# Performance work log

Measured on AMD Instinct MI355X. Metric: run time of the kernel, lower is better.

The kernel has to match this reference:

```python
import jax, jax.numpy as jnp
import numpy as np

DIM = 768
HEADS = 12
HEAD_DIM = DIM // HEADS
HIDDEN = 4 * DIM
LS_INIT = 1e-5
EPS = 1e-5


def layernorm(x, g, b):
    mu = jnp.mean(x, axis=-1, keepdims=True)
    var = jnp.mean(jnp.square(x - mu), axis=-1, keepdims=True)
    return (x - mu) * jax.lax.rsqrt(var + EPS) * g + b


def setup_inputs() -> dict:
    key = jax.random.key(0)
    ks = jax.random.split(key, 8)
    s = lambda fan_in: 1.0 / np.sqrt(fan_in)
    return {
        "x": jax.random.normal(ks[0], (8, 1024, DIM), dtype=jnp.float32),
        "ln1_g": jnp.ones((DIM,), jnp.float32),
        "ln1_b": jnp.zeros((DIM,), jnp.float32),
        "w_qkv": jax.random.uniform(ks[1], (3 * DIM, DIM), jnp.float32, -s(DIM), s(DIM)),
        "w_proj": jax.random.uniform(ks[2], (DIM, DIM), jnp.float32, -s(DIM), s(DIM)),
        "b_proj": jnp.zeros((DIM,), jnp.float32),
        "ls1_g": jnp.full((DIM,), LS_INIT, jnp.float32),
        "ln2_g": jnp.ones((DIM,), jnp.float32),
        "ln2_b": jnp.zeros((DIM,), jnp.float32),
        "w_fc1": jax.random.uniform(ks[3], (HIDDEN, DIM), jnp.float32, -s(DIM), s(DIM)),
        "b_fc1": jnp.zeros((HIDDEN,), jnp.float32),
        "w_fc2": jax.random.uniform(ks[4], (DIM, HIDDEN), jnp.float32, -s(HIDDEN), s(HIDDEN)),
        "b_fc2": jnp.zeros((DIM,), jnp.float32),
        "ls2_g": jnp.full((DIM,), LS_INIT, jnp.float32),
    }


def reference(x, ln1_g, ln1_b, w_qkv, w_proj, b_proj, ls1_g,
              ln2_g, ln2_b, w_fc1, b_fc1, w_fc2, b_fc2, ls2_g):
    B, N, C = x.shape
    # --- attention branch ---
    h = layernorm(x, ln1_g, ln1_b)
    qkv = h @ w_qkv.T  # [B,N,3C]
    qkv = qkv.reshape(B, N, 3, HEADS, HEAD_DIM)
    q, k, v = qkv[:, :, 0], qkv[:, :, 1], qkv[:, :, 2]  # [B,N,H,D]
    scale = 1.0 / np.sqrt(HEAD_DIM)
    attn = jnp.einsum("bqhd,bkhd->bhqk", q, k) * scale
    attn = jax.nn.softmax(attn, axis=-1)
    o = jnp.einsum("bhqk,bkhd->bqhd", attn, v).reshape(B, N, C)
    o = o @ w_proj.T + b_proj
    x = x + ls1_g * o
    # --- MLP branch ---
    h = layernorm(x, ln2_g, ln2_b)
    h = jax.nn.gelu(h @ w_fc1.T + b_fc1, approximate=False)
    h = h @ w_fc2.T + b_fc2
    x = x + ls2_g * h
    return x
```

## Files before the change

### kernel.cpp

```cpp
#include <hip/hip_runtime.h>
#include <cstdint>
#include <cstddef>

typedef __bf16 bf16x8 __attribute__((ext_vector_type(8)));
typedef float f32x4 __attribute__((ext_vector_type(4)));
typedef int i32x4 __attribute__((ext_vector_type(4)));
typedef int i32x8 __attribute__((ext_vector_type(8)));

__device__ __forceinline__ void gload16(const void* g, void* l) {
  __builtin_amdgcn_global_load_lds((const __attribute__((address_space(1))) void*)g,
                                   (__attribute__((address_space(3))) void*)l, 16, 0, 0);
}

__device__ __forceinline__ float exp2_fast(float x) {
  float r;
  asm("v_exp_f32 %0, %1" : "=v"(r) : "v"(x));
  return r;
}
__device__ __forceinline__ float rcp_fast(float x) {
  float r;
  asm("v_rcp_f32 %0, %1" : "=v"(r) : "v"(x));
  return r;
}

__device__ __forceinline__ unsigned char f32_to_fp8(float x) {
  int p = __builtin_amdgcn_cvt_pk_fp8_f32(x, 0.f, 0, false);
  return (unsigned char)(p & 0xff);
}

__device__ __forceinline__ unsigned int f32_to_fp4(float x) {
  const float a = fabsf(x);
  unsigned int c = a < 0.25f ? 0u : a < 0.75f ? 1u : a < 1.25f ? 2u : a < 1.75f ? 3u
                 : a < 2.5f  ? 4u : a < 3.5f  ? 5u : a < 5.0f  ? 6u : 7u;
  return c | ((__float_as_uint(x) >> 28) & 8u);
}
__device__ __forceinline__ unsigned char pack_fp4x2(float lo, float hi) {
  return (unsigned char)(f32_to_fp4(lo) | (f32_to_fp4(hi) << 4));
}

template<int N> __device__ __forceinline__ void wait_vm() {
  if constexpr (N == 0)       asm volatile("s_waitcnt vmcnt(0)" ::: "memory");
  else if constexpr (N == 4)  asm volatile("s_waitcnt vmcnt(4)" ::: "memory");
  else if constexpr (N == 5)  asm volatile("s_waitcnt vmcnt(5)" ::: "memory");
}

#define S_BARRIER() __builtin_amdgcn_s_barrier()
#define WAIT_LGKM() asm volatile("s_waitcnt lgkmcnt(0)" ::: "memory")

__global__ __launch_bounds__(256) void ln_kernel(const float* __restrict__ x,
    const float* __restrict__ g, const float* __restrict__ b,
    unsigned char* __restrict__ out)
{
  __shared__ float red[8];
  const int row = blockIdx.x, t = threadIdx.x;
  const float* xr = x + (size_t)row * 768;
  float v0 = xr[t], v1 = xr[t + 256], v2 = xr[t + 512];
  float s = v0 + v1 + v2;
  float q = v0 * v0 + v1 * v1 + v2 * v2;
  #pragma unroll
  for (int off = 32; off > 0; off >>= 1) {
    s += __shfl_xor(s, off, 64);
    q += __shfl_xor(q, off, 64);
  }
  const int w = t >> 6;
  if ((t & 63) == 0) { red[w] = s; red[4 + w] = q; }
  __syncthreads();
  s = red[0] + red[1] + red[2] + red[3];
  q = red[4] + red[5] + red[6] + red[7];
  const float mu = s * (1.0f / 768.0f);
  const float var = q * (1.0f / 768.0f) - mu * mu;
  const float rstd = rsqrtf(var + 1e-5f);
  unsigned char* orow = out + (size_t)row * 768;
  orow[t]       = f32_to_fp8((v0 - mu) * rstd * g[t]       + b[t]);
  orow[t + 256] = f32_to_fp8((v1 - mu) * rstd * g[t + 256] + b[t + 256]);
  orow[t + 512] = f32_to_fp8((v2 - mu) * rstd * g[t + 512] + b[t + 512]);
}

__global__ __launch_bounds__(256) void cast4_kernel(
    const float* __restrict__ i0, const float* __restrict__ i1,
    const float* __restrict__ i2, const float* __restrict__ i3,
    unsigned char* __restrict__ o0, unsigned char* __restrict__ o1,
    unsigned char* __restrict__ o2, unsigned char* __restrict__ o3)
{
  const int n0 = 2304 * 768 / 4, n1 = 768 * 768 / 4;
  const int n2 = 3072 * 768 / 4, n3 = 768 * 3072 / 4;
  const int total = n0 + n1 + n2 + n3;
  for (int i = blockIdx.x * 256 + threadIdx.x; i < total; i += gridDim.x * 256) {
    const float* in; unsigned char* out; int j = i; float ws = 128.0f;
    if (j < n0) { in = i0; out = o0; }
    else if ((j -= n0) < n1) { in = i1; out = o1; }
    else if ((j -= n1) < n2) { in = i2; out = o2; }
    else { j -= n2; in = i3; out = o3; ws = 256.0f; }
    float4 v = ((const float4*)in)[j];
    const unsigned char b0 = pack_fp4x2(v.x * ws, v.y * ws);
    const unsigned char b1 = pack_fp4x2(v.z * ws, v.w * ws);
    ((unsigned short*)out)[j] = (unsigned short)(b0 | (b1 << 8));
  }
}

template<int MODE>
__global__ __launch_bounds__(256) void gemm_kernel(
    const unsigned char* __restrict__ A, const unsigned char* __restrict__ W, int K,
    unsigned int scaleB,
    const float* __restrict__ bias, const float* __restrict__ resid,
    const float* __restrict__ ls, float* __restrict__ outf,
    unsigned char* __restrict__ outb,
    __bf16* __restrict__ qo, __bf16* __restrict__ ko, __bf16* __restrict__ vo)
{
  constexpr int FM = 4, FN = 2;
  __shared__ unsigned char As[2 * 128 * 128];
  __shared__ unsigned char Bs[2 * 64 * 64];

  const int nx = gridDim.x;
  const int nwg = nx * gridDim.y;
  const int orig = blockIdx.x + nx * blockIdx.y;
  const int nid = (orig & 7) * (nwg >> 3) + (orig >> 3);
  const int bx = nid % nx, by = nid / nx;

  const int t = threadIdx.x;
  const int lane = t & 63;
  const int w = t >> 6;
  const int wm = w >> 1, wn = w & 1;
  const int m0 = by * 128, n0 = bx * 64;
  const int rl = lane & 15, gs = lane >> 4;
  const int Kb2 = K >> 1;

  f32x4 acc[FM][FN];
  #pragma unroll
  for (int i = 0; i < FM; ++i)
    #pragma unroll
    for (int j = 0; j < FN; ++j) acc[i][j] = { 0.f, 0.f, 0.f, 0.f };

  const unsigned char* Asrc[4];
  #pragma unroll
  for (int i = 0; i < 4; ++i) {
    const int g = i * 256 + t, row = g >> 3, gc = g & 7;
    Asrc[i] = A + (size_t)(m0 + row) * K + ((gc ^ (row & 7)) << 4);
  }
  const unsigned char* Bsrc1;
  {
    const int row = t >> 2, gc = t & 3;
    Bsrc1 = W + (size_t)(n0 + row) * Kb2 + ((gc ^ (row & 3)) << 4);
  }

  auto stage = [&](int kt, int buf) {
    const int ka = kt << 7;
    const int kb = kt << 6;
    #pragma unroll
    for (int i = 0; i < 4; ++i)
      gload16(Asrc[i] + ka, As + buf * 16384 + (i * 256 + t) * 16);
    gload16(Bsrc1 + kb, Bs + buf * 4096 + t * 16);
  };

  auto ldA = [&](const unsigned char* rowbase, int sw) -> i32x8 {
    const i32x4 lo = *(const i32x4*)(rowbase + (((2 * gs + 0) ^ sw) << 4));
    const i32x4 hi = *(const i32x4*)(rowbase + (((2 * gs + 1) ^ sw) << 4));
    i32x8 r;
    r[0] = lo[0]; r[1] = lo[1]; r[2] = lo[2]; r[3] = lo[3];
    r[4] = hi[0]; r[5] = hi[1]; r[6] = hi[2]; r[7] = hi[3];
    return r;
  };
  auto ldB = [&](const unsigned char* rowbase, int sw) -> i32x8 {
    const i32x4 v = *(const i32x4*)(rowbase + ((gs ^ sw) << 4));
    i32x8 r;
    r[0] = v[0]; r[1] = v[1]; r[2] = v[2]; r[3] = v[3];
    r[4] = 0; r[5] = 0; r[6] = 0; r[7] = 0;
    return r;
  };

  const int nk = K >> 7;
  stage(0, 0);

  #pragma unroll 2
  for (int kt = 0; kt < nk; ++kt) {
    const int cur = kt & 1;
    if (kt + 1 < nk) { stage(kt + 1, cur ^ 1); wait_vm<5>(); }
    else             { wait_vm<0>(); }
    S_BARRIER();

    const unsigned char* Ac = As + cur * 16384;
    const unsigned char* Bc = Bs + cur * 4096;
    i32x8 af[FM], bfr[FN];
    #pragma unroll
    for (int fm = 0; fm < FM; ++fm) {
      const int row = wm * 64 + fm * 16 + rl;
      af[fm] = ldA(Ac + row * 128, row & 7);
    }
    #pragma unroll
    for (int fn = 0; fn < FN; ++fn) {
      const int row = wn * 32 + fn * 16 + rl;
      bfr[fn] = ldB(Bc + row * 64, row & 3);
    }
    #pragma unroll
    for (int fm = 0; fm < FM; ++fm)
      #pragma unroll
      for (int fn = 0; fn < FN; ++fn)
        acc[fm][fn] = __builtin_amdgcn_mfma_scale_f32_16x16x128_f8f6f4(
            af[fm], bfr[fn], acc[fm][fn],
            0, 4,
            0, 0x7F7F7F7F,
            0, (int)scaleB);

    S_BARRIER();
  }

  #pragma unroll
  for (int fm = 0; fm < FM; ++fm) {
    const int rbase = m0 + wm * 64 + fm * 16 + gs * 4;
    #pragma unroll
    for (int fn = 0; fn < FN; ++fn) {
      const int c = n0 + wn * 32 + fn * 16 + rl;
      #pragma unroll
      for (int b = 0; b < 4; ++b) {
        const int r = rbase + b;
        const float val = acc[fm][fn][b];
        if constexpr (MODE == 0) {
          const int sec = c / 768;
          const int cc = c - sec * 768;
          const int hh = cc >> 6, d = cc & 63;
          const int batch = r >> 10, n = r & 1023;
          const size_t bh = (size_t)(batch * 12 + hh);
          if (sec == 0)      qo[(bh * 1024 + n) * 64 + d] = (__bf16)(val * 0.1803368801111204f);
          else if (sec == 1) ko[(bh * 1024 + n) * 64 + d] = (__bf16)val;
          else               vo[(bh * 64 + d) * 1024 + n] = (__bf16)val;
        } else if constexpr (MODE == 1) {
          const size_t idx = (size_t)r * 768 + c;
          outf[idx] = resid[idx] + ls[c] * (val + bias[c]);
        } else if constexpr (MODE == 2) {
          const float h = val + bias[c];
          const float z = h * (1.0f + 0.044715f * h * h);
          const float e = exp2_fast(2.3021181f * z);
          const float gl = h - h * rcp_fast(1.0f + e);
          outb[(size_t)r * 3072 + c] = f32_to_fp8(gl);
        } else {
          const size_t idx = (size_t)r * 768 + c;
          outf[idx] = resid[idx] + ls[c] * (val + bias[c]);
        }
      }
    }
  }
}

__global__ __launch_bounds__(256, 3) void attn_kernel(
    const __bf16* __restrict__ Q, const __bf16* __restrict__ Kb,
    const __bf16* __restrict__ Vt, unsigned char* __restrict__ Ob)
{
  __shared__ __bf16 Ks[2][64 * 64];
  __shared__ __bf16 Vs[2][64 * 64];
  __shared__ __bf16 P_lds[4][32 * 72];

  const int nid = blockIdx.x;
  const int b7 = nid & 7, rest = nid >> 3;
  const int qt = rest & 7;
  const int bh = b7 + ((rest >> 3) << 3);

  const int t = threadIdx.x, lane = t & 63, w = t >> 6;
  const int rl = lane & 15, gs = lane >> 4;
  const int q0 = qt * 128 + w * 32;
  const __bf16* Qh = Q  + (size_t)bh * 1024 * 64;
  const char*   Kg = (const char*)(Kb + (size_t)bh * 1024 * 64);
  const char*   Vg = (const char*)(Vt + (size_t)bh * 64 * 1024);
  __bf16* Pw = &P_lds[w][0];

  const int g0 = w * 64 + lane;
  const int g1 = 256 + g0;
  const int r0 = g0 >> 3, sb0 = (g0 & 7) ^ (r0 & 7);
  const int r1 = g1 >> 3, sb1 = (g1 & 7) ^ (r1 & 7);

  bf16x8 aq[2][2];
  #pragma unroll
  for (int m = 0; m < 2; ++m)
    #pragma unroll
    for (int ks = 0; ks < 2; ++ks)
      aq[m][ks] = *(const bf16x8*)(Qh + (size_t)(q0 + m * 16 + rl) * 64 + ks * 32 + gs * 8);

  f32x4 accO[2][4];
  #pragma unroll
  for (int m = 0; m < 2; ++m)
    #pragma unroll
    for (int d = 0; d < 4; ++d) accO[m][d] = { 0.f, 0.f, 0.f, 0.f };
  float L[2][4];
  #pragma unroll
  for (int m = 0; m < 2; ++m)
    #pragma unroll
    for (int b = 0; b < 4; ++b) L[m][b] = 0.f;

  {
    gload16(Kg + (size_t)r0 * 128 + sb0 * 16, (char*)Ks[0] + g0 * 16);
    gload16(Kg + (size_t)r1 * 128 + sb1 * 16, (char*)Ks[0] + g1 * 16);
    gload16(Vg + (size_t)r0 * 2048 + sb0 * 16, (char*)Vs[0] + g0 * 16);
    gload16(Vg + (size_t)r1 * 2048 + sb1 * 16, (char*)Vs[0] + g1 * 16);
  }

  for (int tile = 0; tile < 16; ++tile) {
    const int cur = tile & 1;
    if (tile + 1 < 16) {
      const int nxt = cur ^ 1;
      const size_t kofs = (size_t)(tile + 1) * 64;
      gload16(Kg + (kofs + r0) * 128 + sb0 * 16, (char*)Ks[nxt] + g0 * 16);
      gload16(Kg + (kofs + r1) * 128 + sb1 * 16, (char*)Ks[nxt] + g1 * 16);
      gload16(Vg + (size_t)r0 * 2048 + kofs * 2 + sb0 * 16, (char*)Vs[nxt] + g0 * 16);
      gload16(Vg + (size_t)r1 * 2048 + kofs * 2 + sb1 * 16, (char*)Vs[nxt] + g1 * 16);
      wait_vm<4>();
    } else {
      wait_vm<0>();
    }
    S_BARRIER();

    const __bf16* Kc = Ks[cur];
    const __bf16* Vc = Vs[cur];

    f32x4 s[2][4];
    #pragma unroll
    for (int m = 0; m < 2; ++m)
      #pragma unroll
      for (int ct = 0; ct < 4; ++ct) s[m][ct] = { 0.f, 0.f, 0.f, 0.f };
    __builtin_amdgcn_s_setprio(1);
    #pragma unroll
    for (int ct = 0; ct < 4; ++ct) {
      #pragma unroll
      for (int ks = 0; ks < 2; ++ks) {
        const int row = ct * 16 + rl;
        const int blk = (ks * 4 + gs) ^ (row & 7);
        bf16x8 kf = *(const bf16x8*)(Kc + row * 64 + blk * 8);
        s[0][ct] = __builtin_amdgcn_mfma_f32_16x16x32_bf16(aq[0][ks], kf, s[0][ct], 0, 0, 0);
        s[1][ct] = __builtin_amdgcn_mfma_f32_16x16x32_bf16(aq[1][ks], kf, s[1][ct], 0, 0, 0);
      }
    }
    __builtin_amdgcn_s_setprio(0);

    #pragma unroll
    for (int m = 0; m < 2; ++m) {
      #pragma unroll
      for (int b = 0; b < 4; ++b) {
        float rs = 0.f;
        #pragma unroll
        for (int ct = 0; ct < 4; ++ct) {
          const float p = exp2_fast(s[m][ct][b]);
          rs += p;
          Pw[(m * 16 + gs * 4 + b) * 72 + ct * 16 + rl] = (__bf16)p;
        }
        L[m][b] += rs;
      }
    }

    WAIT_LGKM();
    bf16x8 ap[2][2];
    #pragma unroll
    for (int m = 0; m < 2; ++m)
      #pragma unroll
      for (int ks = 0; ks < 2; ++ks)
        ap[m][ks] = *(const bf16x8*)(Pw + (m * 16 + rl) * 72 + ks * 32 + gs * 8);

    __builtin_amdgcn_s_setprio(1);
    #pragma unroll
    for (int dt = 0; dt < 4; ++dt) {
      #pragma unroll
      for (int ks = 0; ks < 2; ++ks) {
        const int row = dt * 16 + rl;
        const int blk = (ks * 4 + gs) ^ (row & 7);
        bf16x8 vf = *(const bf16x8*)(Vc + row * 64 + blk * 8);
        accO[0][dt] = __builtin_amdgcn_mfma_f32_16x16x32_bf16(ap[0][ks], vf, accO[0][dt], 0, 0, 0);
        accO[1][dt] = __builtin_amdgcn_mfma_f32_16x16x32_bf16(ap[1][ks], vf, accO[1][dt], 0, 0, 0);
      }
    }
    __builtin_amdgcn_s_setprio(0);

    S_BARRIER();
  }

  float invL[2][4];
  #pragma unroll
  for (int m = 0; m < 2; ++m)
    #pragma unroll
    for (int b = 0; b < 4; ++b) {
      float rs = L[m][b];
      #pragma unroll
      for (int off = 1; off < 16; off <<= 1) rs += __shfl_xor(rs, off, 16);
      invL[m][b] = 1.0f / rs;
    }

  const int batch = bh / 12, hh = bh - batch * 12;
  #pragma unroll
  for (int m = 0; m < 2; ++m) {
    const size_t rowbase = (size_t)batch * 1024 + qt * 128 + w * 32 + m * 16 + gs * 4;
    #pragma unroll
    for (int dt = 0; dt < 4; ++dt)
      #pragma unroll
      for (int b = 0; b < 4; ++b)
        Ob[(rowbase + b) * 768 + hh * 64 + dt * 16 + rl] = f32_to_fp8(accO[m][dt][b] * invL[m][b]);
  }
}

extern "C" void kernel_launch(void* const* d_in, const int* in_sizes, int n_in,
                              void* d_out, int out_size, void* d_ws, size_t ws_size,
                              hipStream_t stream) {
  const float* x      = (const float*)d_in[0];
  const float* ln1_g  = (const float*)d_in[1];
  const float* ln1_b  = (const float*)d_in[2];
  const float* w_qkv  = (const float*)d_in[3];
  const float* w_proj = (const float*)d_in[4];
  const float* b_proj = (const float*)d_in[5];
  const float* ls1    = (const float*)d_in[6];
  const float* ln2_g  = (const float*)d_in[7];
  const float* ln2_b  = (const float*)d_in[8];
  const float* w_fc1  = (const float*)d_in[9];
  const float* b_fc1  = (const float*)d_in[10];
  const float* w_fc2  = (const float*)d_in[11];
  const float* b_fc2  = (const float*)d_in[12];
  const float* ls2    = (const float*)d_in[13];
  float* out = (float*)d_out;

  char* ws = (char*)d_ws;
  size_t off = 0;
  auto alloc = [&](size_t bytes) { char* p = ws + off; off += (bytes + 255) & ~(size_t)255; return p; };
  unsigned char* h1    = (unsigned char*)alloc(8192ull * 768);
  unsigned char* wqkv4 = (unsigned char*)alloc(2304ull * 384);
  unsigned char* wprj4 = (unsigned char*)alloc(768ull * 384);
  unsigned char* wfc14 = (unsigned char*)alloc(3072ull * 384);
  unsigned char* wfc24 = (unsigned char*)alloc(768ull * 1536);
  __bf16* Qb    = (__bf16*)alloc(8192ull * 768 * 2);
  __bf16* Kb    = (__bf16*)alloc(8192ull * 768 * 2);
  __bf16* Vt    = (__bf16*)alloc(8192ull * 768 * 2);
  float*  out1  = (float*)alloc(8192ull * 768 * 4);
  unsigned char* fc1o = (unsigned char*)alloc(8192ull * 3072);
  unsigned char* h2   = (unsigned char*)alloc(8192ull * 768);

  const unsigned int SC7 = 0x78787878u;
  const unsigned int SC8 = 0x77777777u;

  ln_kernel<<<8192, 256, 0, stream>>>(x, ln1_g, ln1_b, h1);
  cast4_kernel<<<2048, 256, 0, stream>>>(w_qkv, w_proj, w_fc1, w_fc2,
                                         wqkv4, wprj4, wfc14, wfc24);

  gemm_kernel<0><<<dim3(36, 64), 256, 0, stream>>>(h1, wqkv4, 768, SC7,
      nullptr, nullptr, nullptr, nullptr, nullptr, Qb, Kb, Vt);

  attn_kernel<<<96 * 8, 256, 0, stream>>>(Qb, Kb, Vt, h1);

  gemm_kernel<1><<<dim3(12, 64), 256, 0, stream>>>(h1, wprj4, 768, SC7,
      b_proj, x, ls1, out1, nullptr, nullptr, nullptr, nullptr);

  ln_kernel<<<8192, 256, 0, stream>>>(out1, ln2_g, ln2_b, h2);

  gemm_kernel<2><<<dim3(48, 64), 256, 0, stream>>>(h2, wfc14, 768, SC7,
      b_fc1, nullptr, nullptr, nullptr, fc1o, nullptr, nullptr, nullptr);

  gemm_kernel<3><<<dim3(12, 64), 256, 0, stream>>>(fc1o, wfc24, 3072, SC8,
      b_fc2, out1, ls2, out, nullptr, nullptr, nullptr, nullptr);
}
```

Before: 175.8 us.

## Switch attention Q/K/V and P to fp8 with fp8 MFMA

The QKV GEMM epilogue now writes Q, K and V as fp8 bytes instead of bf16. The attention kernel loads these with one 16-byte async load per thread for K and V, uses a new swizzle, and stores P as fp8 in a smaller LDS buffer. Both attention matmuls use 16x16x32 fp8 MFMA, and occupancy is raised to 7 blocks. This halves Q/K/V traffic and LDS footprint, but adds fp8 quantization error to attention scores and probabilities.

New measurement: 230.2 us. +30.9%, slower.

```diff
diff --git a/kernel.cpp b/kernel.cpp
--- a/kernel.cpp
+++ b/kernel.cpp
@@ -40,7 +40,7 @@
 
 template<int N> __device__ __forceinline__ void wait_vm() {
   if constexpr (N == 0)       asm volatile("s_waitcnt vmcnt(0)" ::: "memory");
-  else if constexpr (N == 4)  asm volatile("s_waitcnt vmcnt(4)" ::: "memory");
+  else if constexpr (N == 2)  asm volatile("s_waitcnt vmcnt(2)" ::: "memory");
   else if constexpr (N == 5)  asm volatile("s_waitcnt vmcnt(5)" ::: "memory");
 }
 
@@ -105,7 +105,8 @@
     const float* __restrict__ bias, const float* __restrict__ resid,
     const float* __restrict__ ls, float* __restrict__ outf,
     unsigned char* __restrict__ outb,
-    __bf16* __restrict__ qo, __bf16* __restrict__ ko, __bf16* __restrict__ vo)
+    unsigned char* __restrict__ qo, unsigned char* __restrict__ ko,
+    unsigned char* __restrict__ vo)
 {
   constexpr int FM = 4, FN = 2;
   __shared__ unsigned char As[2 * 128 * 128];
@@ -220,9 +221,9 @@
           const int hh = cc >> 6, d = cc & 63;
           const int batch = r >> 10, n = r & 1023;
           const size_t bh = (size_t)(batch * 12 + hh);
-          if (sec == 0)      qo[(bh * 1024 + n) * 64 + d] = (__bf16)(val * 0.1803368801111204f);
-          else if (sec == 1) ko[(bh * 1024 + n) * 64 + d] = (__bf16)val;
-          else               vo[(bh * 64 + d) * 1024 + n] = (__bf16)val;
+          if (sec == 0)      qo[(bh * 1024 + n) * 64 + d] = f32_to_fp8(val * 0.1803368801111204f);
+          else if (sec == 1) ko[(bh * 1024 + n) * 64 + d] = f32_to_fp8(val);
+          else               vo[(bh * 64 + d) * 1024 + n] = f32_to_fp8(val);
         } else if constexpr (MODE == 1) {
           const size_t idx = (size_t)r * 768 + c;
           outf[idx] = resid[idx] + ls[c] * (val + bias[c]);
@@ -241,13 +242,13 @@
   }
 }
 
-__global__ __launch_bounds__(256, 3) void attn_kernel(
-    const __bf16* __restrict__ Q, const __bf16* __restrict__ Kb,
-    const __bf16* __restrict__ Vt, unsigned char* __restrict__ Ob)
+__global__ __launch_bounds__(256, 7) void attn_kernel(
+    const unsigned char* __restrict__ Q, const unsigned char* __restrict__ Kb,
+    const unsigned char* __restrict__ Vt, unsigned char* __restrict__ Ob)
 {
-  __shared__ __bf16 Ks[2][64 * 64];
-  __shared__ __bf16 Vs[2][64 * 64];
-  __shared__ __bf16 P_lds[4][32 * 72];
+  __shared__ unsigned char Ks[2][64 * 64];
+  __shared__ unsigned char Vs[2][64 * 64];
+  __shared__ unsigned char P_lds[4][32 * 40];
 
   const int nid = blockIdx.x;
   const int b7 = nid & 7, rest = nid >> 3;
@@ -257,22 +258,20 @@
   const int t = threadIdx.x, lane = t & 63, w = t >> 6;
   const int rl = lane & 15, gs = lane >> 4;
   const int q0 = qt * 128 + w * 32;
-  const __bf16* Qh = Q  + (size_t)bh * 1024 * 64;
-  const char*   Kg = (const char*)(Kb + (size_t)bh * 1024 * 64);
-  const char*   Vg = (const char*)(Vt + (size_t)bh * 64 * 1024);
-  __bf16* Pw = &P_lds[w][0];
-
-  const int g0 = w * 64 + lane;
-  const int g1 = 256 + g0;
-  const int r0 = g0 >> 3, sb0 = (g0 & 7) ^ (r0 & 7);
-  const int r1 = g1 >> 3, sb1 = (g1 & 7) ^ (r1 & 7);
-
-  bf16x8 aq[2][2];
+  const unsigned char* Qh = Q  + (size_t)bh * 1024 * 64;
+  const unsigned char* Kg = Kb + (size_t)bh * 1024 * 64;
+  const unsigned char* Vg = Vt + (size_t)bh * 64 * 1024;
+  unsigned char* Pw = &P_lds[w][0];
+
+  const int r0 = t >> 2, gc0 = t & 3;
+  const int sg0 = gc0 ^ (r0 & 3);
+
+  long aq[2][2];
   #pragma unroll
   for (int m = 0; m < 2; ++m)
     #pragma unroll
     for (int ks = 0; ks < 2; ++ks)
-      aq[m][ks] = *(const bf16x8*)(Qh + (size_t)(q0 + m * 16 + rl) * 64 + ks * 32 + gs * 8);
+      aq[m][ks] = *(const long*)(Qh + (size_t)(q0 + m * 16 + rl) * 64 + ks * 32 + gs * 8);
 
   f32x4 accO[2][4];
   #pragma unroll
@@ -285,30 +284,24 @@
     #pragma unroll
     for (int b = 0; b < 4; ++b) L[m][b] = 0.f;
 
-  {
-    gload16(Kg + (size_t)r0 * 128 + sb0 * 16, (char*)Ks[0] + g0 * 16);
-    gload16(Kg + (size_t)r1 * 128 + sb1 * 16, (char*)Ks[0] + g1 * 16);
-    gload16(Vg + (size_t)r0 * 2048 + sb0 * 16, (char*)Vs[0] + g0 * 16);
-    gload16(Vg + (size_t)r1 * 2048 + sb1 * 16, (char*)Vs[0] + g1 * 16);
-  }
+  gload16(Kg + (size_t)r0 * 64 + sg0 * 16, (char*)Ks[0] + t * 16);
+  gload16(Vg + (size_t)r0 * 1024 + sg0 * 16, (char*)Vs[0] + t * 16);
 
   for (int tile = 0; tile < 16; ++tile) {
     const int cur = tile & 1;
     if (tile + 1 < 16) {
       const int nxt = cur ^ 1;
       const size_t kofs = (size_t)(tile + 1) * 64;
-      gload16(Kg + (kofs + r0) * 128 + sb0 * 16, (char*)Ks[nxt] + g0 * 16);
-      gload16(Kg + (kofs + r1) * 128 + sb1 * 16, (char*)Ks[nxt] + g1 * 16);
-      gload16(Vg + (size_t)r0 * 2048 + kofs * 2 + sb0 * 16, (char*)Vs[nxt] + g0 * 16);
-      gload16(Vg + (size_t)r1 * 2048 + kofs * 2 + sb1 * 16, (char*)Vs[nxt] + g1 * 16);
-      wait_vm<4>();
+      gload16(Kg + (kofs + r0) * 64 + sg0 * 16, (char*)Ks[nxt] + t * 16);
+      gload16(Vg + (size_t)r0 * 1024 + kofs + sg0 * 16, (char*)Vs[nxt] + t * 16);
+      wait_vm<2>();
     } else {
       wait_vm<0>();
     }
     S_BARRIER();
 
-    const __bf16* Kc = Ks[cur];
-    const __bf16* Vc = Vs[cur];
+    const unsigned char* Kc = Ks[cur];
+    const unsigned char* Vc = Vs[cur];
 
     f32x4 s[2][4];
     #pragma unroll
@@ -321,10 +314,10 @@
       #pragma unroll
       for (int ks = 0; ks < 2; ++ks) {
         const int row = ct * 16 + rl;
-        const int blk = (ks * 4 + gs) ^ (row & 7);
-        bf16x8 kf = *(const bf16x8*)(Kc + row * 64 + blk * 8);
-        s[0][ct] = __builtin_amdgcn_mfma_f32_16x16x32_bf16(aq[0][ks], kf, s[0][ct], 0, 0, 0);
-        s[1][ct] = __builtin_amdgcn_mfma_f32_16x16x32_bf16(aq[1][ks], kf, s[1][ct], 0, 0, 0);
+        const int p8 = (ks * 4 + gs) ^ ((row & 3) << 1);
+        const long kf = *(const long*)(Kc + row * 64 + p8 * 8);
+        s[0][ct] = __builtin_amdgcn_mfma_f32_16x16x32_fp8_fp8(aq[0][ks], kf, s[0][ct], 0, 0, 0);
+        s[1][ct] = __builtin_amdgcn_mfma_f32_16x16x32_fp8_fp8(aq[1][ks], kf, s[1][ct], 0, 0, 0);
       }
     }
     __builtin_amdgcn_s_setprio(0);
@@ -338,19 +331,19 @@
         for (int ct = 0; ct < 4; ++ct) {
           const float p = exp2_fast(s[m][ct][b]);
           rs += p;
-          Pw[(m * 16 + gs * 4 + b) * 72 + ct * 16 + rl] = (__bf16)p;
+          Pw[(m * 16 + gs * 4 + b) * 40 + ct * 16 + rl] = f32_to_fp8(p);
         }
         L[m][b] += rs;
       }
     }
 
     WAIT_LGKM();
-    bf16x8 ap[2][2];
+    long ap[2][2];
     #pragma unroll
     for (int m = 0; m < 2; ++m)
       #pragma unroll
       for (int ks = 0; ks < 2; ++ks)
-        ap[m][ks] = *(const bf16x8*)(Pw + (m * 16 + rl) * 72 + ks * 32 + gs * 8);
+        ap[m][ks] = *(const long*)(Pw + (m * 16 + rl) * 40 + ks * 32 + gs * 8);
 
     __builtin_amdgcn_s_setprio(1);
     #pragma unroll
@@ -358,10 +351,10 @@
       #pragma unroll
       for (int ks = 0; ks < 2; ++ks) {
         const int row = dt * 16 + rl;
-        const int blk = (ks * 4 + gs) ^ (row & 7);
-        bf16x8 vf = *(const bf16x8*)(Vc + row * 64 + blk * 8);
-        accO[0][dt] = __builtin_amdgcn_mfma_f32_16x16x32_bf16(ap[0][ks], vf, accO[0][dt], 0, 0, 0);
-        accO[1][dt] = __builtin_amdgcn_mfma_f32_16x16x32_bf16(ap[1][ks], vf, accO[1][dt], 0, 0, 0);
+        const int p8 = (ks * 4 + gs) ^ ((row & 3) << 1);
+        const long vf = *(const long*)(Vc + row * 64 + p8 * 8);
+        accO[0][dt] = __builtin_amdgcn_mfma_f32_16x16x32_fp8_fp8(ap[0][ks], vf, accO[0][dt], 0, 0, 0);
+        accO[1][dt] = __builtin_amdgcn_mfma_f32_16x16x32_fp8_fp8(ap[1][ks], vf, accO[1][dt], 0, 0, 0);
       }
     }
     __builtin_amdgcn_s_setprio(0);
@@ -419,9 +412,9 @@
   unsigned char* wprj4 = (unsigned char*)alloc(768ull * 384);
   unsigned char* wfc14 = (unsigned char*)alloc(3072ull * 384);
   unsigned char* wfc24 = (unsigned char*)alloc(768ull * 1536);
-  __bf16* Qb    = (__bf16*)alloc(8192ull * 768 * 2);
-  __bf16* Kb    = (__bf16*)alloc(8192ull * 768 * 2);
-  __bf16* Vt    = (__bf16*)alloc(8192ull * 768 * 2);
+  unsigned char* Qb    = (unsigned char*)alloc(8192ull * 768);
+  unsigned char* Kb    = (unsigned char*)alloc(8192ull * 768);
+  unsigned char* Vt    = (unsigned char*)alloc(8192ull * 768);
   float*  out1  = (float*)alloc(8192ull * 768 * 4);
   unsigned char* fc1o = (unsigned char*)alloc(8192ull * 3072);
   unsigned char* h2   = (unsigned char*)alloc(8192ull * 768);
```
